# Kernel optimization log

Hardware: AMD Instinct MI355X
Metric: run time of the kernel (lower is better)

Reference implementation:

```python
import jax, jax.numpy as jnp
import numpy as np

N = 20000
E = 640000


def setup_inputs() -> dict:
    key = jax.random.key(0)
    k1, k2, k3, k4 = jax.random.split(key, 4)
    IN, H, C = 4096, 512, 10
    x = jax.random.normal(k1, (N, IN), dtype=jnp.float32)
    edge_index = jax.random.randint(k2, (2, E), 0, N, dtype=jnp.int64)
    W1 = jax.random.normal(k3, (IN, H), dtype=jnp.float32) * (1.0 / np.sqrt(IN))
    b1 = jnp.zeros((H,), dtype=jnp.float32)
    W2 = jax.random.normal(k4, (H, C), dtype=jnp.float32) * (1.0 / np.sqrt(H))
    b2 = jnp.zeros((C,), dtype=jnp.float32)
    return {"x": x, "edge_index": edge_index, "W1": W1, "b1": b1, "W2": W2, "b2": b2}


def _gcn_conv(x, src, dst, W, b):
    # Dense transform first (PyG GCNConv does XW then propagate).
    h = x @ W  # [N, F_out]
    # Add self loops.
    loops = jnp.arange(N, dtype=src.dtype)
    s = jnp.concatenate([src, loops])
    d = jnp.concatenate([dst, loops])
    # Symmetric normalization D^{-1/2} (A+I) D^{-1/2}; degree counted on dst.
    deg = jax.ops.segment_sum(jnp.ones_like(d, dtype=h.dtype), d, num_segments=N)
    dinv = jnp.where(deg > 0, jax.lax.rsqrt(deg), 0.0)
    norm = dinv[s] * dinv[d]  # [E+N]
    msg = h[s] * norm[:, None]  # gather + scale
    out = jax.ops.segment_sum(msg, d, num_segments=N)  # scatter-add aggregate
    return out + b


def reference(x, edge_index, W1, b1, W2, b2):
    src, dst = edge_index[0], edge_index[1]
    h = _gcn_conv(x, src, dst, W1, b1)  # conv1 (dropout disabled / eval)
    h = jax.nn.relu(h)
    h = _gcn_conv(h, src, dst, W2, b2)  # conv2
    return jax.nn.log_softmax(h, axis=1)
```

## Files before the change

kernel.cpp:

```cpp
#include <hip/hip_runtime.h>
#include <cstdint>
#include <cstddef>

#define NN  20000
#define EE  640000
#define KIN 4096
#define HD  512
#define NC  10
#define CAP 128

typedef __attribute__((ext_vector_type(8))) short short8;
typedef __attribute__((ext_vector_type(4))) float f32x4;

__device__ __forceinline__ unsigned short f2b(float f) {
  union { float f; unsigned int u; } v; v.f = f;
  unsigned int r = v.u + 0x7fffu + ((v.u >> 16) & 1u);
  return (unsigned short)(r >> 16);
}

__device__ __forceinline__ unsigned int cvt2(float lo, float hi) {
  unsigned int r;
  asm("v_cvt_pk_bf16_f32 %0, %1, %2" : "=v"(r) : "v"(lo), "v"(hi));
  return r;
}

__device__ __forceinline__ void gload16(const void* g, void* l) {
  __builtin_amdgcn_global_load_lds(
      (const __attribute__((address_space(1))) unsigned int*)g,
      (__attribute__((address_space(3))) unsigned int*)l, 16, 0, 0);
}

__global__ __launch_bounds__(256) void scatk(const int* __restrict__ src, const int* __restrict__ dst,
                                             int* __restrict__ deg, int* __restrict__ csr) {
  int e = blockIdx.x * 256 + threadIdx.x;
  if (e < EE) {
    int d = dst[e];
    int p = atomicAdd(&deg[d], 1);
    csr[d * CAP + p] = src[e];
  }
}

__global__ __launch_bounds__(256) void dinvk(const int* __restrict__ deg, float* __restrict__ dinv) {
  int i = blockIdx.x * 256 + threadIdx.x;
  if (i < NN) dinv[i] = 1.0f / sqrtf((float)(deg[i] + 1));
}

__global__ __launch_bounds__(256) void transk(const float* __restrict__ W1, unsigned short* __restrict__ w1t) {
  __shared__ float tile[32][33];
  int h0 = blockIdx.x * 32;
  int k0 = blockIdx.y * 32;
  int tx = threadIdx.x & 31, ty = threadIdx.x >> 5;
#pragma unroll
  for (int r = 0; r < 4; ++r) {
    int k = ty * 4 + r;
    tile[k][tx] = W1[(size_t)(k0 + k) * HD + h0 + tx];
  }
  __syncthreads();
#pragma unroll
  for (int r = 0; r < 4; ++r) {
    int h = ty * 4 + r;
    w1t[(size_t)(h0 + h) * KIN + k0 + tx] = f2b(tile[tx][h]);
  }
}

__global__ __launch_bounds__(256) void gemm1(const float* __restrict__ x,
                                             const unsigned short* __restrict__ w1t,
                                             unsigned short* __restrict__ h1b) {
  __shared__ __align__(16) unsigned short As[128 * 64];
  __shared__ __align__(16) unsigned short Bs[128 * 64];
  int t = threadIdx.x;
  int l = t & 63, w = t >> 6;
  int wm = w >> 1, wn = w & 1;

  int orig = blockIdx.x;
  int xcd = orig & 7, jj = orig >> 3;
  int tile = (xcd < 4 ? xcd * 79 : 316 + (xcd - 4) * 78) + jj;
  int bm = (tile >> 2) * 128;
  int bn = (tile & 3) * 128;

  int stRow = t >> 3;
  int stQ = (t & 7) ^ (stRow & 7);
  const float* ga[4];
#pragma unroll
  for (int i = 0; i < 4; ++i) {
    int m = bm + i * 32 + stRow;
    if (m > NN - 1) m = NN - 1;
    ga[i] = x + (size_t)m * KIN + stQ * 8;
  }

  int rl = l >> 3;
  int cq = (l & 7) ^ rl;
  const unsigned short* gb[4];
  unsigned short* lB[4];
#pragma unroll
  for (int i = 0; i < 4; ++i) {
    int rowB = bn + i * 32 + w * 8 + rl;
    gb[i] = w1t + (size_t)rowB * KIN + cq * 8;
    lB[i] = Bs + (i * 32 + w * 8) * 64;
  }

  int col0 = ((l >> 4) ^ (l & 7));
  int fm[4], fn[4];
#pragma unroll
  for (int i = 0; i < 4; ++i) fm[i] = (wm * 64 + i * 16 + (l & 15)) * 64 + col0 * 8;
#pragma unroll
  for (int j = 0; j < 4; ++j) fn[j] = (wn * 64 + j * 16 + (l & 15)) * 64 + col0 * 8;

  f32x4 acc[4][4] = {};

  for (int kt = 0; kt < KIN / 64; ++kt) {
    int k0 = kt * 64;
    __syncthreads();
#pragma unroll
    for (int i = 0; i < 4; ++i) gload16(gb[i] + k0, lB[i]);
#pragma unroll
    for (int i = 0; i < 4; ++i) {
      float4 a0 = *reinterpret_cast<const float4*>(ga[i] + k0);
      float4 a1 = *reinterpret_cast<const float4*>(ga[i] + k0 + 4);
      uint4 val;
      val.x = cvt2(a0.x, a0.y);
      val.y = cvt2(a0.z, a0.w);
      val.z = cvt2(a1.x, a1.y);
      val.w = cvt2(a1.z, a1.w);
      *reinterpret_cast<uint4*>(As + i * 2048 + 8 * t) = val;
    }
    __syncthreads();
#pragma unroll
    for (int kk = 0; kk < 2; ++kk) {
      int xr = kk << 5;
      short8 af[4], bf[4];
#pragma unroll
      for (int i = 0; i < 4; ++i) af[i] = *reinterpret_cast<const short8*>(As + (fm[i] ^ xr));
#pragma unroll
      for (int j = 0; j < 4; ++j) bf[j] = *reinterpret_cast<const short8*>(Bs + (fn[j] ^ xr));
#pragma unroll
      for (int i = 0; i < 4; ++i)
#pragma unroll
        for (int j = 0; j < 4; ++j)
          acc[i][j] = __builtin_amdgcn_mfma_f32_16x16x32_bf16(af[i], bf[j], acc[i][j], 0, 0, 0);
    }
  }

  int lq = l >> 4;
  bool even = (l & 1) == 0;
#pragma unroll
  for (int i = 0; i < 4; ++i) {
    int row0 = bm + wm * 64 + i * 16 + lq * 4;
#pragma unroll
    for (int j = 0; j < 4; ++j) {
      int col = bn + wn * 64 + j * 16 + (l & 15);
#pragma unroll
      for (int r = 0; r < 4; ++r) {
        float v0 = acc[i][j][r];
        float v1 = __shfl_xor(v0, 1);
        int row = row0 + r;
        if (even && row < NN) {
          *reinterpret_cast<unsigned int*>(h1b + (size_t)row * HD + col) = cvt2(v0, v1);
        }
      }
    }
  }
}

__global__ __launch_bounds__(256) void sgk(const unsigned short* __restrict__ h1b, const int* __restrict__ deg,
                                           const int* __restrict__ csr, const float* __restrict__ dinv,
                                           const float* __restrict__ b1, const float* __restrict__ W2,
                                           float* __restrict__ h2) {
  __shared__ int s_idx[CAP];
  __shared__ float s_w[CAP];
  __shared__ float red[4][NC];
  int i = blockIdx.x;
  int c = threadIdx.x;
  float di = dinv[i];
  int dg = deg[i];
  if (c < dg) {
    int s = csr[i * CAP + c];
    s_idx[c] = s;
    s_w[c] = dinv[s] * di;
  }
  const unsigned int* h1v = reinterpret_cast<const unsigned int*>(h1b);
  unsigned int su = h1v[(size_t)i * 256 + c];
  float wself = di * di;
  float a0 = __uint_as_float(su << 16) * wself;
  float a1 = __uint_as_float(su & 0xffff0000u) * wself;
  __syncthreads();
#pragma unroll 4
  for (int jj = 0; jj < dg; ++jj) {
    unsigned int u = h1v[(size_t)s_idx[jj] * 256 + c];
    float wgt = s_w[jj];
    a0 += __uint_as_float(u << 16) * wgt;
    a1 += __uint_as_float(u & 0xffff0000u) * wgt;
  }
  float2 bb = reinterpret_cast<const float2*>(b1)[c];
  float zx = fmaxf(a0 + bb.x, 0.f);
  float zy = fmaxf(a1 + bb.y, 0.f);
  const float* w2r = W2 + (size_t)(2 * c) * NC;
  float part[NC];
#pragma unroll
  for (int cc = 0; cc < NC; ++cc) part[cc] = zx * w2r[cc] + zy * w2r[NC + cc];
#pragma unroll
  for (int cc = 0; cc < NC; ++cc) {
#pragma unroll
    for (int m = 1; m < 64; m <<= 1) part[cc] += __shfl_xor(part[cc], m, 64);
  }
  int wv = c >> 6, ln = c & 63;
  if (ln == 0) {
#pragma unroll
    for (int cc = 0; cc < NC; ++cc) red[wv][cc] = part[cc];
  }
  __syncthreads();
  if (c < NC) h2[(size_t)i * NC + c] = red[0][c] + red[1][c] + red[2][c] + red[3][c];
}

__global__ __launch_bounds__(64) void spmm2(const float* __restrict__ h2, const int* __restrict__ deg,
                                            const int* __restrict__ csr, const float* __restrict__ dinv,
                                            const float* __restrict__ b2, float* __restrict__ out) {
  int i = blockIdx.x;
  int l = threadIdx.x;
  float di = dinv[i];
  int dg = deg[i];
  float acc[NC] = {};
  for (int e = l; e < dg; e += 64) {
    int s = csr[i * CAP + e];
    float wgt = dinv[s] * di;
    const float2* hp = reinterpret_cast<const float2*>(h2 + (size_t)s * NC);
#pragma unroll
    for (int cc = 0; cc < 5; ++cc) {
      float2 v = hp[cc];
      acc[2 * cc] += v.x * wgt;
      acc[2 * cc + 1] += v.y * wgt;
    }
  }
  if (l == 0) {
    float ws = di * di;
#pragma unroll
    for (int cc = 0; cc < NC; ++cc) acc[cc] += h2[(size_t)i * NC + cc] * ws;
  }
#pragma unroll
  for (int cc = 0; cc < NC; ++cc) {
#pragma unroll
    for (int m = 1; m < 64; m <<= 1) acc[cc] += __shfl_xor(acc[cc], m, 64);
  }
  if (l == 0) {
    float v[NC];
    float mx = -1e30f;
#pragma unroll
    for (int cc = 0; cc < NC; ++cc) {
      v[cc] = acc[cc] + b2[cc];
      mx = fmaxf(mx, v[cc]);
    }
    float s = 0.f;
#pragma unroll
    for (int cc = 0; cc < NC; ++cc) s += expf(v[cc] - mx);
    float lse = mx + logf(s);
#pragma unroll
    for (int cc = 0; cc < NC; ++cc) out[(size_t)i * NC + cc] = v[cc] - lse;
  }
}

extern "C" void kernel_launch(void* const* d_in, const int* in_sizes, int n_in,
                              void* d_out, int out_size, void* d_ws, size_t ws_size,
                              hipStream_t stream) {
  (void)in_sizes; (void)n_in; (void)out_size; (void)ws_size;
  const float* x  = (const float*)d_in[0];
  const int*   ei = (const int*)d_in[1];
  const float* W1 = (const float*)d_in[2];
  const float* b1 = (const float*)d_in[3];
  const float* W2 = (const float*)d_in[4];
  const float* b2 = (const float*)d_in[5];
  float* out = (float*)d_out;
  char* ws = (char*)d_ws;

  unsigned short* w1t = (unsigned short*)(ws);
  unsigned short* h1b = (unsigned short*)(ws + 4194304);
  float* h2   = (float*)(ws + 24674304);
  int*   deg  = (int*)(ws + 25474304);
  float* dinv = (float*)(ws + 25554304);
  int*   csr  = (int*)(ws + 25634304);

  const int* srcp = ei;
  const int* dstp = ei + EE;

  hipMemsetAsync(deg, 0, NN * sizeof(int), stream);
  scatk<<<(EE + 255) / 256, 256, 0, stream>>>(srcp, dstp, deg, csr);
  dinvk<<<(NN + 255) / 256, 256, 0, stream>>>(deg, dinv);
  transk<<<dim3(16, 128), 256, 0, stream>>>(W1, w1t);
  gemm1<<<157 * 4, 256, 0, stream>>>(x, w1t, h1b);
  sgk<<<NN, 256, 0, stream>>>(h1b, deg, csr, dinv, b1, W2, h2);
  spmm2<<<NN, 64, 0, stream>>>(h2, deg, csr, dinv, b2, out);
}
```

Baseline: 689.5 us.

## Double-buffer LDS tiles in gemm1 to overlap global loads with MFMA

Splits the A and B shared-memory tiles into two buffers and prefetches the next K-tile while MFMAs run on the current one. The next A tile is held in registers, then converted to bf16 and written after compute, and B goes straight to LDS through gload16. This cuts the two barriers per iteration to one and hides global memory latency behind compute. In exchange it doubles LDS use to 64KB per block and adds registers for the prefetched floats, which can lower occupancy.

```diff
diff --git a/kernel.cpp b/kernel.cpp
--- a/kernel.cpp
+++ b/kernel.cpp
@@ -66,8 +66,8 @@
 __global__ __launch_bounds__(256) void gemm1(const float* __restrict__ x,
                                              const unsigned short* __restrict__ w1t,
                                              unsigned short* __restrict__ h1b) {
-  __shared__ __align__(16) unsigned short As[128 * 64];
-  __shared__ __align__(16) unsigned short Bs[128 * 64];
+  __shared__ __align__(16) unsigned short As[2][128 * 64];
+  __shared__ __align__(16) unsigned short Bs[2][128 * 64];
   int t = threadIdx.x;
   int l = t & 63, w = t >> 6;
   int wm = w >> 1, wn = w & 1;
@@ -91,12 +91,12 @@
   int rl = l >> 3;
   int cq = (l & 7) ^ rl;
   const unsigned short* gb[4];
-  unsigned short* lB[4];
+  int lBoff[4];
 #pragma unroll
   for (int i = 0; i < 4; ++i) {
     int rowB = bn + i * 32 + w * 8 + rl;
     gb[i] = w1t + (size_t)rowB * KIN + cq * 8;
-    lB[i] = Bs + (i * 32 + w * 8) * 64;
+    lBoff[i] = (i * 32 + w * 8) * 64;
   }
 
   int col0 = ((l >> 4) ^ (l & 7));
@@ -107,37 +107,63 @@
   for (int j = 0; j < 4; ++j) fn[j] = (wn * 64 + j * 16 + (l & 15)) * 64 + col0 * 8;
 
   f32x4 acc[4][4] = {};
-
-  for (int kt = 0; kt < KIN / 64; ++kt) {
-    int k0 = kt * 64;
-    __syncthreads();
-#pragma unroll
-    for (int i = 0; i < 4; ++i) gload16(gb[i] + k0, lB[i]);
-#pragma unroll
-    for (int i = 0; i < 4; ++i) {
-      float4 a0 = *reinterpret_cast<const float4*>(ga[i] + k0);
-      float4 a1 = *reinterpret_cast<const float4*>(ga[i] + k0 + 4);
-      uint4 val;
-      val.x = cvt2(a0.x, a0.y);
-      val.y = cvt2(a0.z, a0.w);
-      val.z = cvt2(a1.x, a1.y);
-      val.w = cvt2(a1.z, a1.w);
-      *reinterpret_cast<uint4*>(As + i * 2048 + 8 * t) = val;
-    }
-    __syncthreads();
+  float4 pa[4][2];
+
+#pragma unroll
+  for (int i = 0; i < 4; ++i) {
+    pa[i][0] = *reinterpret_cast<const float4*>(ga[i]);
+    pa[i][1] = *reinterpret_cast<const float4*>(ga[i] + 4);
+  }
+#pragma unroll
+  for (int i = 0; i < 4; ++i) gload16(gb[i], &Bs[0][lBoff[i]]);
+#pragma unroll
+  for (int i = 0; i < 4; ++i) {
+    uint4 val;
+    val.x = cvt2(pa[i][0].x, pa[i][0].y);
+    val.y = cvt2(pa[i][0].z, pa[i][0].w);
+    val.z = cvt2(pa[i][1].x, pa[i][1].y);
+    val.w = cvt2(pa[i][1].z, pa[i][1].w);
+    *reinterpret_cast<uint4*>(&As[0][i * 2048 + 8 * t]) = val;
+  }
+  __syncthreads();
+
+  for (int tk = 0; tk < 64; ++tk) {
+    int cur = tk & 1;
+    int k1 = (tk + 1) * 64;
+    if (tk < 63) {
+#pragma unroll
+      for (int i = 0; i < 4; ++i) {
+        pa[i][0] = *reinterpret_cast<const float4*>(ga[i] + k1);
+        pa[i][1] = *reinterpret_cast<const float4*>(ga[i] + k1 + 4);
+      }
+#pragma unroll
+      for (int i = 0; i < 4; ++i) gload16(gb[i] + k1, &Bs[cur ^ 1][lBoff[i]]);
+    }
 #pragma unroll
     for (int kk = 0; kk < 2; ++kk) {
       int xr = kk << 5;
       short8 af[4], bf[4];
 #pragma unroll
-      for (int i = 0; i < 4; ++i) af[i] = *reinterpret_cast<const short8*>(As + (fm[i] ^ xr));
-#pragma unroll
-      for (int j = 0; j < 4; ++j) bf[j] = *reinterpret_cast<const short8*>(Bs + (fn[j] ^ xr));
+      for (int i = 0; i < 4; ++i) af[i] = *reinterpret_cast<const short8*>(&As[cur][0] + (fm[i] ^ xr));
+#pragma unroll
+      for (int j = 0; j < 4; ++j) bf[j] = *reinterpret_cast<const short8*>(&Bs[cur][0] + (fn[j] ^ xr));
 #pragma unroll
       for (int i = 0; i < 4; ++i)
 #pragma unroll
         for (int j = 0; j < 4; ++j)
           acc[i][j] = __builtin_amdgcn_mfma_f32_16x16x32_bf16(af[i], bf[j], acc[i][j], 0, 0, 0);
+    }
+    if (tk < 63) {
+#pragma unroll
+      for (int i = 0; i < 4; ++i) {
+        uint4 val;
+        val.x = cvt2(pa[i][0].x, pa[i][0].y);
+        val.y = cvt2(pa[i][0].z, pa[i][0].w);
+        val.z = cvt2(pa[i][1].x, pa[i][1].y);
+        val.w = cvt2(pa[i][1].z, pa[i][1].w);
+        *reinterpret_cast<uint4*>(&As[cur ^ 1][i * 2048 + 8 * t]) = val;
+      }
+      __syncthreads();
     }
   }
 
```

After: 758.2 us. 1.1x slower.
